# Performance work log

Measured on AMD Instinct MI355X. Metric: run time of the kernel, lower is better.

The kernel has to match this reference:

```python
import jax, jax.numpy as jnp
import numpy as np

NUM_HEADS = 12
HIDDEN = 768
HEAD_DIM = HIDDEN // NUM_HEADS
WINDOW = 128
LN_EPS = 1e-5


def setup_inputs() -> dict:
    key = jax.random.key(0)
    ks = jax.random.split(key, 12)
    B, S, H = 2048, 2 * WINDOW + 1, HIDDEN
    s = 0.02
    return {
        "hidden_states": jax.random.normal(ks[0], (B, S, H), dtype=jnp.float32),
        "Wq": jax.random.normal(ks[1], (H, H), dtype=jnp.float32) * s,
        "bq": jnp.zeros((H,), jnp.float32),
        "Wk": jax.random.normal(ks[2], (H, H), dtype=jnp.float32) * s,
        "bk": jnp.zeros((H,), jnp.float32),
        "Wv": jax.random.normal(ks[3], (H, H), dtype=jnp.float32) * s,
        "bv": jnp.zeros((H,), jnp.float32),
        "Wo": jax.random.normal(ks[4], (H, H), dtype=jnp.float32) * s,
        "bo": jnp.zeros((H,), jnp.float32),
        "pe_w": jax.random.normal(ks[5], (H, 1), dtype=jnp.float32) * s,
        "pe_b": jnp.zeros((H,), jnp.float32),
        "ln_g": jnp.ones((H,), jnp.float32),
        "ln_b": jnp.zeros((H,), jnp.float32),
        "pos_bias": jax.random.normal(ks[6], (1, NUM_HEADS, 1, 2 * WINDOW + 1), dtype=jnp.float32) * s,
    }


def _layernorm(x, g, b):
    mu = jnp.mean(x, axis=-1, keepdims=True)
    var = jnp.mean(jnp.square(x - mu), axis=-1, keepdims=True)
    return (x - mu) * jax.lax.rsqrt(var + LN_EPS) * g + b


def reference(hidden_states, Wq, bq, Wk, bk, Wv, bv, Wo, bo, pe_w, pe_b, ln_g, ln_b, pos_bias):
    B, S, H = hidden_states.shape
    mid = S // 2
    # relative positions -> learned position encoding (Linear(1,H) + LayerNorm)
    pos = ((jnp.arange(S, dtype=jnp.float32) - mid) / (mid + 1e-6))[:, None]  # [S,1]
    pe = _layernorm(pos @ pe_w.T + pe_b, ln_g, ln_b)  # [S,H]
    hs = hidden_states + pe[None]  # [B,S,H]
    # single middle-token query, full-window keys/values
    q = (hs[:, mid] @ Wq.T + bq).reshape(B, NUM_HEADS, HEAD_DIM)      # [B,h,d]
    k = (hs @ Wk.T + bk).reshape(B, S, NUM_HEADS, HEAD_DIM)           # [B,S,h,d]
    v = (hs @ Wv.T + bv).reshape(B, S, NUM_HEADS, HEAD_DIM)
    scores = jnp.einsum("bhd,bshd->bhs", q, k) / np.sqrt(HEAD_DIM)    # [B,h,S]
    scores = scores + pos_bias[0, :, 0, :S][None]                      # additive learned bias
    probs = jax.nn.softmax(scores, axis=-1)
    ctx = jnp.einsum("bhs,bshd->bhd", probs, v).reshape(B, H)         # [B,H]
    out = (ctx @ Wo.T + bo)[:, None, :]                               # [B,1,H]
    return out
```

## Files before the change

### kernel.cpp

```cpp
#include <hip/hip_runtime.h>
#include <hip/hip_bf16.h>
#include <math.h>

#define NH   12
#define HD   64
#define HDIM 768
#define SEQ  257
#define MIDP 128
#define BTOT 2048
#define CTP  18

typedef __attribute__((ext_vector_type(8))) short short8;
typedef __attribute__((ext_vector_type(4))) float f32x4;

__device__ inline unsigned short f2bf(float x){
  union { float f; unsigned u; } v; v.f = x;
  unsigned r = v.u + 0x7FFFu + ((v.u >> 16) & 1u);
  return (unsigned short)(r >> 16);
}
__device__ inline float bf2f(unsigned short h){
  union { unsigned u; float f; } v; v.u = ((unsigned)h) << 16; return v.f;
}
__device__ inline unsigned cvt2(float lo, float hi){
  union { __hip_bfloat162 h; unsigned u; } z;
  z.h = __float22bfloat162_rn(make_float2(lo, hi));
  return z.u;
}
__device__ inline float dot4(float4 a, float4 b){
  return fmaf(a.x,b.x, fmaf(a.y,b.y, fmaf(a.z,b.z, a.w*b.w)));
}
__device__ inline void barrier_lds(){
  __builtin_amdgcn_sched_barrier(0);
  asm volatile("s_waitcnt lgkmcnt(0)" ::: "memory");
  __builtin_amdgcn_s_barrier();
  __builtin_amdgcn_sched_barrier(0);
}

__global__ __launch_bounds__(256) void k0_pre(
    const float* __restrict__ pe_w, const float* __restrict__ pe_b,
    const float* __restrict__ ln_g, const float* __restrict__ ln_b,
    const float* __restrict__ pos_bias,
    float* __restrict__ pemid, float* __restrict__ alpha, float* __restrict__ beta,
    float* __restrict__ Av, float* __restrict__ Bv, float* __restrict__ Cv,
    float* __restrict__ pbT) {
  __shared__ float red[5][256];
  const int t = threadIdx.x;
  float sw=0.f, sb=0.f, sww=0.f, swb=0.f, sbb=0.f;
  for (int j=t; j<HDIM; j+=256) {
    float w=pe_w[j], b=pe_b[j];
    sw+=w; sb+=b; sww+=w*w; swb+=w*b; sbb+=b*b;
  }
  red[0][t]=sw; red[1][t]=sb; red[2][t]=sww; red[3][t]=swb; red[4][t]=sbb;
  __syncthreads();
  for (int off=128; off>0; off>>=1) {
    if (t<off) {
      red[0][t]+=red[0][t+off]; red[1][t]+=red[1][t+off]; red[2][t]+=red[2][t+off];
      red[3][t]+=red[3][t+off]; red[4][t]+=red[4][t+off];
    }
    __syncthreads();
  }
  const float inv = 1.0f/(float)HDIM;
  const float mw=red[0][0]*inv, mc=red[1][0]*inv;
  const float Vw =red[2][0]*inv - mw*mw;
  const float Cwc=red[3][0]*inv - mw*mc;
  const float Vc =red[4][0]*inv - mc*mc;
  for (int s=t; s<288; s+=256) {
    if (s < SEQ) {
      float pos = (float)(s - MIDP) / ((float)MIDP + 1e-6f);
      float var = pos*pos*Vw + 2.f*pos*Cwc + Vc;
      float rstd = rsqrtf(var + 1e-5f);
      alpha[s] = pos*rstd; beta[s] = rstd;
    } else { alpha[s] = 0.f; beta[s] = 0.f; }
  }
  const float rstd0 = rsqrtf(Vc + 1e-5f);
  for (int j=t; j<HDIM; j+=256) {
    float g = ln_g[j];
    Av[j] = (pe_w[j]-mw)*g;
    Bv[j] = (pe_b[j]-mc)*g;
    Cv[j] = ln_b[j];
    pemid[j] = (pe_b[j]-mc)*rstd0*g + ln_b[j];
  }
  for (int i=t; i<288*16; i+=256) {
    int s = i>>4, h = i&15;
    pbT[i] = (s<SEQ && h<NH) ? pos_bias[h*SEQ+s] : 0.f;
  }
}

__global__ __launch_bounds__(256) void gemm64_bf(
    const float* __restrict__ A, long lda, long aoffz,
    const float* __restrict__ Bm, long ldb, long boffz, int bT,
    float* __restrict__ C, long ldc, long coffz,
    int K,
    const float* __restrict__ bias, long biasoffz,
    const float* __restrict__ avec, float scale) {
  __shared__ __align__(16) unsigned short Asb[64*40];
  __shared__ __align__(16) unsigned short Bsb[64*40];
  const int t   = threadIdx.x;
  const int l15 = t & 15;
  const int lg  = (t >> 4) & 3;
  const int w   = t >> 6;
  const int z   = blockIdx.z;
  const long n0 = (long)blockIdx.y * 64;
  A  += (long)blockIdx.x*64*lda + (long)z*aoffz;
  Bm += (long)z*boffz;
  C  += (long)blockIdx.x*64*ldc + n0 + (long)z*coffz;

  const int srow = t >> 2;
  const int skk  = (t & 3) * 8;
  const int kB   = t >> 3;
  const int nB   = (t & 7) * 8;

  f32x4 acc[4];
  #pragma unroll
  for (int i=0;i<4;i++){ f32x4 zz={0.f,0.f,0.f,0.f}; acc[i]=zz; }

  for (int k0 = 0; k0 < K; k0 += 32) {
    {
      const float* p = &A[(long)srow*lda + k0 + skk];
      float4 a0 = *(const float4*)p, a1 = *(const float4*)(p+4);
      if (avec) {
        float4 v0 = *(const float4*)&avec[k0+skk], v1 = *(const float4*)&avec[k0+skk+4];
        a0.x+=v0.x; a0.y+=v0.y; a0.z+=v0.z; a0.w+=v0.w;
        a1.x+=v1.x; a1.y+=v1.y; a1.z+=v1.z; a1.w+=v1.w;
      }
      uint4 pk; pk.x=cvt2(a0.x,a0.y); pk.y=cvt2(a0.z,a0.w);
      pk.z=cvt2(a1.x,a1.y); pk.w=cvt2(a1.z,a1.w);
      *(uint4*)&Asb[srow*40 + (skk ^ ((srow&3)<<3))] = pk;
    }
    if (bT) {
      const float* p = &Bm[(long)(n0+srow)*ldb + k0 + skk];
      float4 b0 = *(const float4*)p, b1 = *(const float4*)(p+4);
      uint4 pk; pk.x=cvt2(b0.x,b0.y); pk.y=cvt2(b0.z,b0.w);
      pk.z=cvt2(b1.x,b1.y); pk.w=cvt2(b1.z,b1.w);
      *(uint4*)&Bsb[srow*40 + (skk ^ ((srow&3)<<3))] = pk;
    } else {
      const float* p = &Bm[(long)(k0+kB)*ldb + n0 + nB];
      float4 b0 = *(const float4*)p, b1 = *(const float4*)(p+4);
      const float bv[8] = {b0.x,b0.y,b0.z,b0.w,b1.x,b1.y,b1.z,b1.w};
      #pragma unroll
      for (int i=0;i<8;i++) {
        const int n = nB + i;
        Bsb[n*40 + (kB ^ ((n&3)<<3))] = f2bf(bv[i]);
      }
    }
    __syncthreads();
    union { uint4 q; short8 s8; } af;
    const int arow = w*16 + l15;
    af.q = *(const uint4*)&Asb[arow*40 + ((lg*8) ^ ((arow&3)<<3))];
    #pragma unroll
    for (int nt=0; nt<4; ++nt) {
      union { uint4 q; short8 s8; } bf_;
      const int brow = nt*16 + l15;
      bf_.q = *(const uint4*)&Bsb[brow*40 + ((lg*8) ^ ((brow&3)<<3))];
      acc[nt] = __builtin_amdgcn_mfma_f32_16x16x32_bf16(af.s8, bf_.s8, acc[nt], 0, 0, 0);
    }
    __syncthreads();
  }
  #pragma unroll
  for (int nt=0; nt<4; ++nt) {
    const int col = nt*16 + l15;
    const float bsv = bias ? bias[(long)z*biasoffz + n0 + col] : 0.f;
    #pragma unroll
    for (int r=0; r<4; ++r)
      C[(long)(w*16 + lg*4 + r)*ldc + col] = (acc[nt][r] + bsv)*scale;
  }
}

__global__ __launch_bounds__(256) void kp(
    const float* __restrict__ q, const float* __restrict__ u, const float* __restrict__ bk,
    const float* __restrict__ Av, const float* __restrict__ Bv, const float* __restrict__ Cv,
    float* __restrict__ ca, float* __restrict__ cb, float* __restrict__ cc, int nb) {
  const int wid = blockIdx.x*4 + (threadIdx.x >> 6);
  const int lane = threadIdx.x & 63;
  if (wid >= nb*NH) return;
  const int b = wid / NH, h = wid % NH;
  const float* up = u + (long)b*(NH*HDIM) + h*HDIM;
  float pa=0.f, pb_=0.f, pc=0.f;
  #pragma unroll
  for (int e=0;e<3;e++) {
    int c4 = (lane + 64*e)*4;
    float4 uu = *(const float4*)&up[c4];
    pa += dot4(uu, *(const float4*)&Av[c4]);
    pb_+= dot4(uu, *(const float4*)&Bv[c4]);
    pc += dot4(uu, *(const float4*)&Cv[c4]);
  }
  if (lane < 16) {
    float4 qq = *(const float4*)&q[(long)b*HDIM + h*HD + lane*4];
    float4 bb = *(const float4*)&bk[h*HD + lane*4];
    pc += dot4(qq, bb);
  }
  #pragma unroll
  for (int mlog=0; mlog<6; mlog++) {
    int msk = 1<<mlog;
    pa += __shfl_xor(pa, msk);
    pb_+= __shfl_xor(pb_, msk);
    pc += __shfl_xor(pc, msk);
  }
  if (lane == 0) { ca[wid]=pa; cb[wid]=pb_; cc[wid]=pc; }
}

__global__ __launch_bounds__(256, 2) void k3_v8(
    const float* __restrict__ hs, int b0,
    const float* __restrict__ u,
    const float* __restrict__ ca, const float* __restrict__ cb, const float* __restrict__ cc,
    const float* __restrict__ alpha, const float* __restrict__ beta,
    const float* __restrict__ Av, const float* __restrict__ Bv, const float* __restrict__ Cv,
    const float* __restrict__ pbT, float* __restrict__ mout) {
  const int t   = threadIdx.x;
  const int l   = t & 63;
  const int w   = t >> 6;
  const int l15 = l & 15;
  const int lg  = l >> 4;
  const int bb  = blockIdx.x;
  const int b   = b0 + bb;

  __shared__ __align__(16) unsigned short xbuf[12288 + 768*CTP];
  unsigned short* xrow = xbuf;
  unsigned short* colT = xbuf + 12288;
  __shared__ float sred[4][16][17];
  __shared__ __align__(16) unsigned short wlT[16*16];
  __shared__ float hsum[3][16];

  const float* ub = u + (long)bb*(NH*HDIM);
  short8 uf[6];
  #pragma unroll
  for (int kt=0; kt<6; kt++) {
    union { uint4 q; short8 s8; } s; s.q = make_uint4(0,0,0,0);
    if (l15 < NH) {
      const float* p = ub + l15*HDIM + w*192 + kt*32 + lg*8;
      float4 x0 = *(const float4*)p;
      float4 x1 = *(const float4*)(p+4);
      s.q.x = cvt2(x0.x,x0.y); s.q.y = cvt2(x0.z,x0.w);
      s.q.z = cvt2(x1.x,x1.y); s.q.w = cvt2(x1.z,x1.w);
    }
    uf[kt] = s.s8;
  }
  float cah=0.f, cbh=0.f, cch=0.f;
  if (w==0 && l15<NH) { cah=ca[bb*NH+l15]; cbh=cb[bb*NH+l15]; cch=cc[bb*NH+l15]; }

  f32x4 pv[12];
  #pragma unroll
  for (int i=0;i<12;i++){ f32x4 z={0.f,0.f,0.f,0.f}; pv[i]=z; }
  float rs_p=0.f, sa_p=0.f, sb_p=0.f;

  const float* hrow = hs + (long)b*SEQ*HDIM;
  const int rp = t >> 5;
  const int cq = t & 31;
  union { float4 v4[12]; float f[48]; } g;

  #pragma unroll
  for (int rr=0; rr<2; ++rr)
    #pragma unroll
    for (int e=0; e<6; ++e)
      g.v4[rr*6+e] = *(const float4*)&hrow[(long)(rp*2+rr)*HDIM + cq*4 + e*128];
  #pragma unroll
  for (int rr=0; rr<2; ++rr) {
    const int srow = rp*2+rr;
    #pragma unroll
    for (int e=0; e<6; ++e) {
      float4 v = g.v4[rr*6+e];
      uint2 pk; pk.x = cvt2(v.x,v.y); pk.y = cvt2(v.z,v.w);
      const int c = cq*4 + e*128;
      *(uint2*)&xrow[srow*768 + (c ^ ((srow&7)<<3))] = pk;
    }
  }
  #pragma unroll
  for (int e=0; e<6; ++e)
    #pragma unroll
    for (int d=0; d<4; ++d) {
      const int j = cq*4 + e*128 + d;
      unsigned v = cvt2(g.f[e*4+d], g.f[24+e*4+d]);
      *(unsigned*)&colT[j*CTP + rp*2] = v;
    }
  __syncthreads();

  #pragma unroll 1
  for (int c=0; c<17; ++c) {
    if (c < 16) {
      #pragma unroll
      for (int rr=0; rr<2; ++rr) {
        int sg = (c+1)*16 + rp*2 + rr; if (sg > SEQ-1) sg = SEQ-1;
        #pragma unroll
        for (int e=0; e<6; ++e)
          g.v4[rr*6+e] = *(const float4*)&hrow[(long)sg*HDIM + cq*4 + e*128];
      }
    }
    {
      f32x4 acc = {0.f,0.f,0.f,0.f};
      #pragma unroll
      for (int kt=0; kt<6; kt++) {
        const int col = w*192 + kt*32 + lg*8;
        uint4 raw = *(const uint4*)&xrow[l15*768 + (col ^ ((l15&7)<<3))];
        union { uint4 q; short8 s8; } A; A.q = raw;
        acc = __builtin_amdgcn_mfma_f32_16x16x32_bf16(A.s8, uf[kt], acc, 0, 0, 0);
      }
      #pragma unroll
      for (int r=0; r<4; ++r) sred[w][lg*4+r][l15] = acc[r];
    }
    barrier_lds();
    if (w == 0) {
      #pragma unroll
      for (int r=0; r<4; ++r) {
        const int s = lg*4 + r, sg = c*16 + s;
        float S = sred[0][s][l15]+sred[1][s][l15]+sred[2][s][l15]+sred[3][s][l15];
        float al = alpha[sg], be = beta[sg];
        float sc = S + fmaf(cah, al, fmaf(cbh, be, cch)) + pbT[sg*16 + l15];
        float wv = (sg < SEQ && l15 < NH) ? __expf(sc) : 0.f;
        unsigned short wb = f2bf(wv);
        float wr = bf2f(wb);
        rs_p += wr; sa_p = fmaf(wr, al, sa_p); sb_p = fmaf(wr, be, sb_p);
        wlT[l15*16 + s] = wb;
      }
    }
    barrier_lds();
    {
      union { uint4 q; short8 s8; } B; B.q = make_uint4(0,0,0,0);
      if (lg < 2) B.q = *(const uint4*)&wlT[l15*16 + lg*8];
      #pragma unroll
      for (int tau=0; tau<12; ++tau) {
        const int j = w*192 + tau*16 + l15;
        union { uint4 q; short8 s8; } A; A.q = make_uint4(0,0,0,0);
        if (lg < 2) A.q = *(const uint4*)&colT[j*CTP + lg*8];
        pv[tau] = __builtin_amdgcn_mfma_f32_16x16x32_bf16(A.s8, B.s8, pv[tau], 0, 0, 0);
      }
      if (c < 16) {
        #pragma unroll
        for (int rr=0; rr<2; ++rr) {
          const int srow = rp*2+rr;
          #pragma unroll
          for (int e=0; e<6; ++e) {
            float4 v = g.v4[rr*6+e];
            uint2 pk; pk.x = cvt2(v.x,v.y); pk.y = cvt2(v.z,v.w);
            const int cc2 = cq*4 + e*128;
            *(uint2*)&xrow[srow*768 + (cc2 ^ ((srow&7)<<3))] = pk;
          }
        }
      }
    }
    barrier_lds();
    if (c < 16) {
      #pragma unroll
      for (int e=0; e<6; ++e)
        #pragma unroll
        for (int d=0; d<4; ++d) {
          const int j = cq*4 + e*128 + d;
          unsigned v = cvt2(g.f[e*4+d], g.f[24+e*4+d]);
          *(unsigned*)&colT[j*CTP + rp*2] = v;
        }
    }
  }

  if (w == 0) {
    rs_p += __shfl_xor(rs_p,16); rs_p += __shfl_xor(rs_p,32);
    sa_p += __shfl_xor(sa_p,16); sa_p += __shfl_xor(sa_p,32);
    sb_p += __shfl_xor(sb_p,16); sb_p += __shfl_xor(sb_p,32);
    if (l < 16) { hsum[0][l15]=rs_p; hsum[1][l15]=sa_p; hsum[2][l15]=sb_p; }
  }
  __syncthreads();

  float* mlds = (float*)xbuf;
  if (l15 < NH) {
    #pragma unroll
    for (int tau=0; tau<12; ++tau)
      #pragma unroll
      for (int r=0; r<4; ++r) {
        const int j = w*192 + tau*16 + lg*4 + r;
        mlds[l15*772 + j] = pv[tau][r];
      }
  }
  __syncthreads();
  float* mo = mout + (long)bb*(NH*HDIM);
  #pragma unroll
  for (int e=0; e<9; ++e) {
    const int idx = t + 256*e;
    const int h = idx/192, c4 = (idx%192)*4;
    const float invr = 1.0f/hsum[0][h];
    const float fa = hsum[1][h]*invr, fb = hsum[2][h]*invr;
    float4 mv = *(const float4*)&mlds[h*772 + c4];
    float4 av = *(const float4*)&Av[c4];
    float4 bv4 = *(const float4*)&Bv[c4];
    float4 cv4 = *(const float4*)&Cv[c4];
    float4 o;
    o.x = fmaf(mv.x, invr, fmaf(fa, av.x, fmaf(fb, bv4.x, cv4.x)));
    o.y = fmaf(mv.y, invr, fmaf(fa, av.y, fmaf(fb, bv4.y, cv4.y)));
    o.z = fmaf(mv.z, invr, fmaf(fa, av.z, fmaf(fb, bv4.z, cv4.z)));
    o.w = fmaf(mv.w, invr, fmaf(fa, av.w, fmaf(fb, bv4.w, cv4.w)));
    *(float4*)&mo[h*HDIM + c4] = o;
  }
}

extern "C" void kernel_launch(void* const* d_in, const int* in_sizes, int n_in,
                              void* d_out, int out_size, void* d_ws, size_t ws_size,
                              hipStream_t stream) {
  (void)in_sizes; (void)n_in; (void)out_size;
  const float* hs   = (const float*)d_in[0];
  const float* Wq   = (const float*)d_in[1];
  const float* bq   = (const float*)d_in[2];
  const float* Wk   = (const float*)d_in[3];
  const float* bk   = (const float*)d_in[4];
  const float* Wv   = (const float*)d_in[5];
  const float* bv   = (const float*)d_in[6];
  const float* Wo   = (const float*)d_in[7];
  const float* bo   = (const float*)d_in[8];
  const float* pe_w = (const float*)d_in[9];
  const float* pe_b = (const float*)d_in[10];
  const float* ln_g = (const float*)d_in[11];
  const float* ln_b = (const float*)d_in[12];
  const float* pos_bias = (const float*)d_in[13];
  float* out = (float*)d_out;

  float* wsf   = (float*)d_ws;
  float* pemid = wsf;
  float* alpha = pemid + 768;
  float* beta  = alpha + 288;
  float* Avec  = beta  + 288;
  float* Bvec  = Avec  + 768;
  float* Cvec  = Bvec  + 768;
  float* pbT   = Cvec  + 768;
  float* base  = pbT   + 4608;

  const long perB = 768L + 36L + 9216L + 9216L + 768L;
  long availF = (long)(ws_size/4) - 8256;
  long chunkB = (availF > 0) ? (availF / perB) : 0;
  if (chunkB > BTOT) chunkB = BTOT;
  chunkB &= ~63L;
  if (chunkB < 64) chunkB = 64;

  float* qb   = base;
  float* cab  = qb  + chunkB*HDIM;
  float* cbb  = cab + chunkB*NH;
  float* ccb  = cbb + chunkB*NH;
  float* ub   = ccb + chunkB*NH;
  float* mb   = ub  + chunkB*(long)NH*HDIM;
  float* ctxb = mb  + chunkB*(long)NH*HDIM;

  k0_pre<<<dim3(1), dim3(256), 0, stream>>>(pe_w, pe_b, ln_g, ln_b, pos_bias,
                                            pemid, alpha, beta, Avec, Bvec, Cvec, pbT);

  for (long b0 = 0; b0 < BTOT; b0 += chunkB) {
    long cbN = (BTOT - b0 < chunkB) ? (BTOT - b0) : chunkB;
    int mt = (int)(cbN/64);
    gemm64_bf<<<dim3(mt,12,1), dim3(256), 0, stream>>>(
        hs + b0*(long)SEQ*HDIM + (long)MIDP*HDIM, (long)SEQ*HDIM, 0L,
        Wq, (long)HDIM, 0L, 1,
        qb, (long)HDIM, 0L,
        HDIM, bq, 0L, pemid, 0.125f);
    gemm64_bf<<<dim3(mt,12,12), dim3(256), 0, stream>>>(
        qb, (long)HDIM, (long)HD,
        Wk, (long)HDIM, (long)HD*HDIM, 0,
        ub, (long)NH*HDIM, (long)HDIM,
        HD, (const float*)nullptr, 0L, (const float*)nullptr, 1.0f);
    int nw = (int)(cbN*NH);
    kp<<<dim3((nw+3)/4), dim3(256), 0, stream>>>(qb, ub, bk, Avec, Bvec, Cvec,
                                                 cab, cbb, ccb, (int)cbN);
    k3_v8<<<dim3((int)cbN), dim3(256), 0, stream>>>(
        hs, (int)b0, ub, cab, cbb, ccb, alpha, beta, Avec, Bvec, Cvec, pbT, mb);
    gemm64_bf<<<dim3(mt,1,12), dim3(256), 0, stream>>>(
        mb, (long)NH*HDIM, (long)HDIM,
        Wv, (long)HDIM, (long)HD*HDIM, 1,
        ctxb, (long)HDIM, (long)HD,
        HDIM, bv, (long)HD, (const float*)nullptr, 1.0f);
    gemm64_bf<<<dim3(mt,12,1), dim3(256), 0, stream>>>(
        ctxb, (long)HDIM, 0L,
        Wo, (long)HDIM, 0L, 1,
        out + b0*(long)HDIM, (long)HDIM, 0L,
        HDIM, bo, 0L, (const float*)nullptr, 1.0f);
  }
}
```

Before: 575.2 us.

## Double-buffer global prefetch two chunks ahead and drop softmax-weight LDS barrier

The chunk loop now uses two register buffers, so global loads for chunk c+2 are issued while chunk c computes, which hides more memory latency. Every wave now computes the exp weights redundantly in registers and builds the MFMA B operand directly. This removes the wlT LDS round trip and one barrier per chunk. Alpha and beta are staged in LDS and the positional bias is preloaded per chunk. The cost is higher register pressure from the second 48-float buffer, which may lower occupancy or cause spills.

```diff
diff --git a/kernel.cpp b/kernel.cpp
--- a/kernel.cpp
+++ b/kernel.cpp
@@ -218,8 +218,10 @@
   unsigned short* xrow = xbuf;
   unsigned short* colT = xbuf + 12288;
   __shared__ float sred[4][16][17];
-  __shared__ __align__(16) unsigned short wlT[16*16];
+  __shared__ float al_s[288], be_s[288];
   __shared__ float hsum[3][16];
+
+  for (int i=t; i<288; i+=256) { al_s[i]=alpha[i]; be_s[i]=beta[i]; }
 
   const float* ub = u + (long)bb*(NH*HDIM);
   short8 uf[6];
@@ -236,7 +238,7 @@
     uf[kt] = s.s8;
   }
   float cah=0.f, cbh=0.f, cch=0.f;
-  if (w==0 && l15<NH) { cah=ca[bb*NH+l15]; cbh=cb[bb*NH+l15]; cch=cc[bb*NH+l15]; }
+  if (l15 < NH) { cah=ca[bb*NH+l15]; cbh=cb[bb*NH+l15]; cch=cc[bb*NH+l15]; }
 
   f32x4 pv[12];
   #pragma unroll
@@ -246,109 +248,118 @@
   const float* hrow = hs + (long)b*SEQ*HDIM;
   const int rp = t >> 5;
   const int cq = t & 31;
-  union { float4 v4[12]; float f[48]; } g;
-
-  #pragma unroll
-  for (int rr=0; rr<2; ++rr)
-    #pragma unroll
-    for (int e=0; e<6; ++e)
-      g.v4[rr*6+e] = *(const float4*)&hrow[(long)(rp*2+rr)*HDIM + cq*4 + e*128];
-  #pragma unroll
-  for (int rr=0; rr<2; ++rr) {
-    const int srow = rp*2+rr;
-    #pragma unroll
-    for (int e=0; e<6; ++e) {
-      float4 v = g.v4[rr*6+e];
-      uint2 pk; pk.x = cvt2(v.x,v.y); pk.y = cvt2(v.z,v.w);
-      const int c = cq*4 + e*128;
-      *(uint2*)&xrow[srow*768 + (c ^ ((srow&7)<<3))] = pk;
-    }
-  }
-  #pragma unroll
-  for (int e=0; e<6; ++e)
-    #pragma unroll
-    for (int d=0; d<4; ++d) {
-      const int j = cq*4 + e*128 + d;
-      unsigned v = cvt2(g.f[e*4+d], g.f[24+e*4+d]);
-      *(unsigned*)&colT[j*CTP + rp*2] = v;
-    }
+  union GU { float4 v4[12]; float f[48]; };
+  GU gA, gB;
+
+#define LOAD_INTO(G, CI)                                                          \
+  do {                                                                            \
+    _Pragma("unroll")                                                             \
+    for (int rr_=0; rr_<2; ++rr_) {                                               \
+      int sg_ = (CI)*16 + rp*2 + rr_; if (sg_ > SEQ-1) sg_ = SEQ-1;               \
+      _Pragma("unroll")                                                           \
+      for (int e_=0; e_<6; ++e_)                                                  \
+        G.v4[rr_*6+e_] = *(const float4*)&hrow[(long)sg_*HDIM + cq*4 + e_*128];   \
+    }                                                                             \
+  } while(0)
+
+#define STAGE_XROW(G)                                                             \
+  do {                                                                            \
+    _Pragma("unroll")                                                             \
+    for (int rr_=0; rr_<2; ++rr_) {                                               \
+      const int srow_ = rp*2+rr_;                                                 \
+      _Pragma("unroll")                                                           \
+      for (int e_=0; e_<6; ++e_) {                                                \
+        float4 v_ = G.v4[rr_*6+e_];                                               \
+        uint2 pk_; pk_.x = cvt2(v_.x,v_.y); pk_.y = cvt2(v_.z,v_.w);              \
+        const int c_ = cq*4 + e_*128;                                             \
+        *(uint2*)&xrow[srow_*768 + (c_ ^ ((srow_&7)<<3))] = pk_;                  \
+      }                                                                           \
+    }                                                                             \
+  } while(0)
+
+#define STAGE_COLT(G)                                                             \
+  do {                                                                            \
+    _Pragma("unroll")                                                             \
+    for (int e_=0; e_<6; ++e_)                                                    \
+      _Pragma("unroll")                                                           \
+      for (int d_=0; d_<4; ++d_) {                                                \
+        const int j_ = cq*4 + e_*128 + d_;                                        \
+        unsigned v_ = cvt2(G.f[e_*4+d_], G.f[24+e_*4+d_]);                        \
+        *(unsigned*)&colT[j_*CTP + rp*2] = v_;                                    \
+      }                                                                           \
+  } while(0)
+
+#define CHUNK_BODY(CI, GLD, GST, DOLOAD, DOSTAGE)                                 \
+  do {                                                                            \
+    const int ci_ = (CI);                                                         \
+    float pb_r[8];                                                                \
+    if (lg < 2) {                                                                 \
+      _Pragma("unroll")                                                           \
+      for (int e_=0; e_<8; ++e_)                                                  \
+        pb_r[e_] = pbT[(ci_*16 + lg*8 + e_)*16 + l15];                            \
+    }                                                                             \
+    if (DOLOAD) LOAD_INTO(GLD, ci_+2);                                            \
+    {                                                                             \
+      f32x4 acc = {0.f,0.f,0.f,0.f};                                              \
+      _Pragma("unroll")                                                           \
+      for (int kt_=0; kt_<6; kt_++) {                                             \
+        const int col_ = w*192 + kt_*32 + lg*8;                                   \
+        uint4 raw_ = *(const uint4*)&xrow[l15*768 + (col_ ^ ((l15&7)<<3))];       \
+        union { uint4 q; short8 s8; } A_; A_.q = raw_;                            \
+        acc = __builtin_amdgcn_mfma_f32_16x16x32_bf16(A_.s8, uf[kt_], acc, 0,0,0);\
+      }                                                                           \
+      _Pragma("unroll")                                                           \
+      for (int r_=0; r_<4; ++r_) sred[w][lg*4+r_][l15] = acc[r_];                 \
+    }                                                                             \
+    barrier_lds();                               \
+    union { uint4 q; short8 s8; } B_; B_.q = make_uint4(0,0,0,0);                 \
+    if (lg < 2) {                                                                 \
+      _Pragma("unroll")                                                           \
+      for (int e_=0; e_<8; ++e_) {                                                \
+        const int s_ = lg*8 + e_, sg_ = ci_*16 + s_;                              \
+        float S_ = sred[0][s_][l15]+sred[1][s_][l15]+sred[2][s_][l15]+sred[3][s_][l15];\
+        float al_ = al_s[sg_], be_ = be_s[sg_];                                   \
+        float sc_ = S_ + fmaf(cah, al_, fmaf(cbh, be_, cch)) + pb_r[e_];          \
+        float wv_ = (sg_ < SEQ && l15 < NH) ? __expf(sc_) : 0.f;                  \
+        unsigned short wb_ = f2bf(wv_);                                           \
+        B_.s8[e_] = (short)wb_;                                                   \
+        if (w == 0) {                                                             \
+          float wr_ = bf2f(wb_);                                                  \
+          rs_p += wr_; sa_p = fmaf(wr_, al_, sa_p); sb_p = fmaf(wr_, be_, sb_p);  \
+        }                                                                         \
+      }                                                                           \
+    }                                                                             \
+    {                                                                             \
+      _Pragma("unroll")                                                           \
+      for (int tau_=0; tau_<12; ++tau_) {                                         \
+        const int j_ = w*192 + tau_*16 + l15;                                     \
+        union { uint4 q; short8 s8; } A_; A_.q = make_uint4(0,0,0,0);             \
+        if (lg < 2) A_.q = *(const uint4*)&colT[j_*CTP + lg*8];                   \
+        pv[tau_] = __builtin_amdgcn_mfma_f32_16x16x32_bf16(A_.s8, B_.s8, pv[tau_], 0,0,0);\
+      }                                                                           \
+      if (DOSTAGE) STAGE_XROW(GST);          \
+    }                                                                             \
+    barrier_lds();                         \
+    if (DOSTAGE) STAGE_COLT(GST);                       \
+  } while(0)
+
+  LOAD_INTO(gA, 0);
+  LOAD_INTO(gB, 1);
+  STAGE_XROW(gA);
+  STAGE_COLT(gA);
   __syncthreads();
 
   #pragma unroll 1
-  for (int c=0; c<17; ++c) {
-    if (c < 16) {
-      #pragma unroll
-      for (int rr=0; rr<2; ++rr) {
-        int sg = (c+1)*16 + rp*2 + rr; if (sg > SEQ-1) sg = SEQ-1;
-        #pragma unroll
-        for (int e=0; e<6; ++e)
-          g.v4[rr*6+e] = *(const float4*)&hrow[(long)sg*HDIM + cq*4 + e*128];
-      }
-    }
-    {
-      f32x4 acc = {0.f,0.f,0.f,0.f};
-      #pragma unroll
-      for (int kt=0; kt<6; kt++) {
-        const int col = w*192 + kt*32 + lg*8;
-        uint4 raw = *(const uint4*)&xrow[l15*768 + (col ^ ((l15&7)<<3))];
-        union { uint4 q; short8 s8; } A; A.q = raw;
-        acc = __builtin_amdgcn_mfma_f32_16x16x32_bf16(A.s8, uf[kt], acc, 0, 0, 0);
-      }
-      #pragma unroll
-      for (int r=0; r<4; ++r) sred[w][lg*4+r][l15] = acc[r];
-    }
-    barrier_lds();
-    if (w == 0) {
-      #pragma unroll
-      for (int r=0; r<4; ++r) {
-        const int s = lg*4 + r, sg = c*16 + s;
-        float S = sred[0][s][l15]+sred[1][s][l15]+sred[2][s][l15]+sred[3][s][l15];
-        float al = alpha[sg], be = beta[sg];
-        float sc = S + fmaf(cah, al, fmaf(cbh, be, cch)) + pbT[sg*16 + l15];
-        float wv = (sg < SEQ && l15 < NH) ? __expf(sc) : 0.f;
-        unsigned short wb = f2bf(wv);
-        float wr = bf2f(wb);
-        rs_p += wr; sa_p = fmaf(wr, al, sa_p); sb_p = fmaf(wr, be, sb_p);
-        wlT[l15*16 + s] = wb;
-      }
-    }
-    barrier_lds();
-    {
-      union { uint4 q; short8 s8; } B; B.q = make_uint4(0,0,0,0);
-      if (lg < 2) B.q = *(const uint4*)&wlT[l15*16 + lg*8];
-      #pragma unroll
-      for (int tau=0; tau<12; ++tau) {
-        const int j = w*192 + tau*16 + l15;
-        union { uint4 q; short8 s8; } A; A.q = make_uint4(0,0,0,0);
-        if (lg < 2) A.q = *(const uint4*)&colT[j*CTP + lg*8];
-        pv[tau] = __builtin_amdgcn_mfma_f32_16x16x32_bf16(A.s8, B.s8, pv[tau], 0, 0, 0);
-      }
-      if (c < 16) {
-        #pragma unroll
-        for (int rr=0; rr<2; ++rr) {
-          const int srow = rp*2+rr;
-          #pragma unroll
-          for (int e=0; e<6; ++e) {
-            float4 v = g.v4[rr*6+e];
-            uint2 pk; pk.x = cvt2(v.x,v.y); pk.y = cvt2(v.z,v.w);
-            const int cc2 = cq*4 + e*128;
-            *(uint2*)&xrow[srow*768 + (cc2 ^ ((srow&7)<<3))] = pk;
-          }
-        }
-      }
-    }
-    barrier_lds();
-    if (c < 16) {
-      #pragma unroll
-      for (int e=0; e<6; ++e)
-        #pragma unroll
-        for (int d=0; d<4; ++d) {
-          const int j = cq*4 + e*128 + d;
-          unsigned v = cvt2(g.f[e*4+d], g.f[24+e*4+d]);
-          *(unsigned*)&colT[j*CTP + rp*2] = v;
-        }
-    }
-  }
+  for (int cc = 0; cc < 16; cc += 2) {
+    CHUNK_BODY(cc,   gA, gB, (cc+2 <= 16), true);
+    CHUNK_BODY(cc+1, gB, gA, (cc+3 <= 16), true);
+  }
+  CHUNK_BODY(16, gA, gB, false, false);
+
+#undef CHUNK_BODY
+#undef STAGE_COLT
+#undef STAGE_XROW
+#undef LOAD_INTO
 
   if (w == 0) {
     rs_p += __shfl_xor(rs_p,16); rs_p += __shfl_xor(rs_p,32);
```

Result: faster. 528.2 us (-8.2%).
